# Optimization experiments

Measured on AMD Instinct MI355X. Metric: run time of the kernel, lower is better.

Reference implementation:

```python
import jax, jax.numpy as jnp
import numpy as np

NY, NU, NH = 8, 8, 256
T, NB = 2048, 64


def setup_inputs() -> dict:
    key = jax.random.key(0)
    ks = jax.random.split(key, 10)
    return {
        "_y0": jax.random.normal(ks[0], (NB, NY), dtype=jnp.float32),
        "_U": jax.random.normal(ks[1], (T, NB, NU), dtype=jnp.float32),
        "lmbd_cont_real": jax.random.uniform(ks[2], (NH // 2,), dtype=jnp.float32),
        "lmbd_cont_imag": jax.random.uniform(ks[3], (NH // 2,), dtype=jnp.float32),
        "B": jax.random.normal(ks[4], (NH, NU), dtype=jnp.float32) / np.sqrt(NU).astype(np.float32),
        "multiplier_on_B": jnp.zeros((NH,), dtype=jnp.float32),
        "W_y2x": jax.random.normal(ks[5], (NH, NY), dtype=jnp.float32) / np.sqrt(NY).astype(np.float32),
        "b_y2x": jax.random.normal(ks[6], (NH,), dtype=jnp.float32) * 0.01,
        "W_x2y": jax.random.normal(ks[7], (NY, NH), dtype=jnp.float32) / np.sqrt(NH).astype(np.float32),
        "b_x2y": jax.random.normal(ks[8], (NY,), dtype=jnp.float32) * 0.01,
    }


def reference(_y0, _U, lmbd_cont_real, lmbd_cont_imag, B, multiplier_on_B,
              W_y2x, b_y2x, W_x2y, b_x2y):
    H2 = lmbd_cont_real.shape[0]
    # input drive: (T, NB, NH)
    Bu = jnp.einsum('tbu,hu->tbh', _U, B) * jnp.exp(multiplier_on_B)
    # stable complex-conjugate-pair eigenvalues
    r = jnp.exp(-jnp.abs(lmbd_cont_real))
    theta = (jnp.pi / 2) * lmbd_cont_imag
    re = r * jnp.cos(theta)
    im = r * jnp.sin(theta)
    # initial state from y0
    x0 = _y0 @ W_y2x.T + b_y2x  # (NB, NH)

    def step(x, bu):
        x1, x2 = x[:, :H2], x[:, H2:]
        # A = [[diag(re), -diag(im)], [diag(im), diag(re)]]; x <- x A^T + bu
        nx = jnp.concatenate([re * x1 - im * x2, im * x1 + re * x2], axis=1) + bu
        return nx, nx

    _, X = jax.lax.scan(step, x0, Bu)  # X: (T, NB, NH)
    Y = X @ W_x2y.T + b_x2y  # (T, NB, NY)
    return Y
```

## Files before the change

### kernel.cpp

```cpp
#include <hip/hip_runtime.h>
#include <math.h>

#define T_   2048
#define NB_  64
#define NU_  8
#define NY_  8
#define NH_  256
#define H2_  128
#define CCH  64
#define LCH  32

static const float PI_HALF = 1.5707963267948966f;

typedef _Float16 half8  __attribute__((ext_vector_type(8)));
typedef __fp16   fp16x2 __attribute__((ext_vector_type(2)));
typedef float    f32x4  __attribute__((ext_vector_type(4)));

#define OFF_M     16384
#define OFF_CBUF  147456
#define OFF_INIT  4341760

__global__ __launch_bounds__(128) void k_scanM(
    const float* __restrict__ U, const float* __restrict__ bx2y,
    const float* __restrict__ lr, const float* __restrict__ li,
    const float* __restrict__ B, const float* __restrict__ mult,
    const float* __restrict__ Wx2y,
    char* __restrict__ ws, float* __restrict__ c_buf,
    float* __restrict__ Y)
{
    const int bi  = blockIdx.x;
    const int tid = threadIdx.x;

    if (bi < 256) {
        uint32_t* M32 = (uint32_t*)(ws + OFF_M);
        const int R = bi, dlt = R >> 3, y = R & 7;
        const int h = tid;
        const float e = (float)(dlt + 1);
        float r  = expf(-e * fabsf(lr[h]));
        float an = e * PI_HALF * li[h];
        float c = r * cosf(an), sn = r * sinf(an);
        float W1 = Wx2y[y*NH_ + h];
        float W2 = Wx2y[y*NH_ + h + H2_];
        float Mre = fmaf(W1, c,  W2 * sn);
        float Mim = fmaf(W2, c, -W1 * sn);
        union { fp16x2 h2; uint32_t u32; } pk;
        pk.h2 = __builtin_amdgcn_cvt_pkrtz(Mre, Mim);
        M32[R*128 + h] = pk.u32;
        return;
    }

    const int kb  = bi - 256;
    const int k   = kb >> 6;
    const int b   = kb & 63;
    const int h   = tid;
    const int w   = tid >> 6;
    const int l   = tid & 63;
    const int row = l & 15;
    const int kg  = (l >> 4) & 3;

    float4 lam;
    {
        float a_ = fabsf(lr[h]);
        float r_ = expf(-a_);
        float th = PI_HALF * li[h];
        float re = r_ * cosf(th), im = r_ * sinf(th);
        lam = make_float4(re, im, -im, re);
    }
    float B1[NU_], B2[NU_];
    {
        float s1 = expf(mult[h]), s2 = expf(mult[h + H2_]);
        const float4* bp1 = (const float4*)(B + h*NU_);
        const float4* bp2 = (const float4*)(B + (h + H2_)*NU_);
        float4 a0 = bp1[0], a1 = bp1[1], a2 = bp2[0], a3 = bp2[1];
        B1[0]=a0.x*s1; B1[1]=a0.y*s1; B1[2]=a0.z*s1; B1[3]=a0.w*s1;
        B1[4]=a1.x*s1; B1[5]=a1.y*s1; B1[6]=a1.z*s1; B1[7]=a1.w*s1;
        B2[0]=a2.x*s2; B2[1]=a2.y*s2; B2[2]=a2.z*s2; B2[3]=a2.w*s2;
        B2[4]=a3.x*s2; B2[5]=a3.y*s2; B2[6]=a3.z*s2; B2[7]=a3.w*s2;
    }
    half8 wf[4];
    #pragma unroll
    for (int q2 = 0; q2 < 4; q2++) {
        const int q = 4*w + q2;
        union { uint32_t u[4]; half8 h8; } fu;
        if (row < 8) {
            const float4 wa = *(const float4*)(Wx2y + row*NH_ + q*16 + kg*4);
            const float4 wb = *(const float4*)(Wx2y + row*NH_ + q*16 + kg*4 + H2_);
            union { fp16x2 h2; uint32_t u32; } p;
            p.h2 = __builtin_amdgcn_cvt_pkrtz(wa.x, wb.x); fu.u[0] = p.u32;
            p.h2 = __builtin_amdgcn_cvt_pkrtz(wa.y, wb.y); fu.u[1] = p.u32;
            p.h2 = __builtin_amdgcn_cvt_pkrtz(wa.z, wb.z); fu.u[2] = p.u32;
            p.h2 = __builtin_amdgcn_cvt_pkrtz(wa.w, wb.w); fu.u[3] = p.u32;
        } else {
            fu.u[0]=0; fu.u[1]=0; fu.u[2]=0; fu.u[3]=0;
        }
        wf[q2] = fu.h8;
    }
    const float bias = bx2y[tid & 7];

    __shared__ float    uS[LCH*NU_];
    __shared__ _Float16 xS[16*256];
    __shared__ float    pS[4*132];
    uint32_t* xS32 = (uint32_t*)xS;

    if (tid < 64) {
        ((float4*)uS)[tid] =
            *(const float4*)(U + ((size_t)(k*LCH + (tid>>1))*NB_ + b)*NU_ + (tid&1)*4);
    }
    __syncthreads();

    float x1 = 0.f, x2 = 0.f;
    const int g = h >> 2;

    for (int s = 0; s < 2; s++) {
        #pragma unroll 4
        for (int t16 = 0; t16 < 16; t16++) {
            const int t = s*16 + t16;
            float4 u0 = ((const float4*)uS)[2*t+0];
            float4 u1 = ((const float4*)uS)[2*t+1];
            float u[NU_] = {u0.x,u0.y,u0.z,u0.w,u1.x,u1.y,u1.z,u1.w};
            float bu1=0.f, bu2=0.f;
            #pragma unroll
            for (int i = 0; i < NU_; i++) {
                bu1 = fmaf(u[i], B1[i], bu1);
                bu2 = fmaf(u[i], B2[i], bu2);
            }
            float n1 = fmaf(lam.x, x1, fmaf(lam.z, x2, bu1));
            float n2 = fmaf(lam.y, x1, fmaf(lam.w, x2, bu2));
            x1 = n1; x2 = n2;

            union { fp16x2 h2; uint32_t u32; } pk;
            pk.h2 = __builtin_amdgcn_cvt_pkrtz(x1, x2);
            xS32[t16*128 + ((g ^ t16) & 31)*4 + (h & 3)] = pk.u32;
        }
        __syncthreads();

        f32x4 acc = {0.f,0.f,0.f,0.f};
        #pragma unroll
        for (int q2 = 0; q2 < 4; q2++) {
            const int q = 4*w + q2;
            const int p = ((q << 2) + kg) ^ row;
            const half8* ap = (const half8*)(xS + (row << 8) + (p << 3));
            acc = __builtin_amdgcn_mfma_f32_16x16x32_f16(*ap, wf[q2], acc, 0, 0, 0);
        }
        #pragma unroll
        for (int r = 0; r < 4; r++) pS[r*132 + w*64 + l] = acc[r];
        __syncthreads();

        {
            const int t  = tid >> 3, y = tid & 7;
            const int ls = ((t >> 2) << 4) + y;
            const int rg = t & 3;
            float sum = pS[rg*132 + ls] + pS[rg*132 + 64 + ls];
            Y[((size_t)(k*LCH + s*16 + t)*NB_ + b)*NY_ + y] = sum + bias;
        }
    }

    *(float2*)(c_buf + (size_t)(k*NB_ + b)*(H2_*2) + 2*h) = make_float2(x1, x2);
}

__global__ __launch_bounds__(64) void k_prefix(
    const float* __restrict__ y0, const float* __restrict__ Wy2x,
    const float* __restrict__ by2x,
    const float* __restrict__ lr, const float* __restrict__ li,
    const float* __restrict__ c_buf, uint32_t* __restrict__ initT)
{
    const int g = blockIdx.x*64 + threadIdx.x;
    const int b = g >> 7;
    const int h = g & 127;

    float x1 = by2x[h], x2 = by2x[h+H2_];
    #pragma unroll
    for (int y = 0; y < NY_; y++) {
        float yy = y0[b*NY_ + y];
        x1 = fmaf(yy, Wy2x[h*NY_ + y],        x1);
        x2 = fmaf(yy, Wy2x[(h+H2_)*NY_ + y],  x2);
    }

    const float a_  = fabsf(lr[h]);
    const float rL  = expf(-(float)LCH * a_);
    const float thL = (float)LCH * PI_HALF * li[h];
    const float reL = rL * cosf(thL), imL = rL * sinf(thL);

    #pragma unroll 8
    for (int k = 0; k < CCH; k++) {
        float2 c = *(const float2*)(c_buf + (size_t)k*16384 + b*256 + 2*h);
        union { fp16x2 hh; uint32_t u32; } pk;
        pk.hh = __builtin_amdgcn_cvt_pkrtz(x1, x2);
        initT[(size_t)k*8192 + b*128 + h] = pk.u32;
        float n1 = fmaf(reL, x1, fmaf(-imL, x2, c.x));
        float n2 = fmaf(imL, x1, fmaf( reL, x2, c.y));
        x1 = n1; x2 = n2;
    }
}

__global__ __launch_bounds__(256) void k_corr(
    const _Float16* __restrict__ M, const uint32_t* __restrict__ initT,
    float* __restrict__ Y)
{
    const int bi   = blockIdx.x;
    const int k    = bi >> 3;
    const int half = (bi >> 2) & 1;
    const int rtg  = bi & 3;
    const int tid  = threadIdx.x;
    const int w    = tid >> 6, l = tid & 63;
    const int lane16 = l & 15, kg = l >> 4;

    __shared__ _Float16 bS[32*264];
    {
        uint32_t* bS32 = (uint32_t*)bS;
        const int r = tid >> 3, seg = tid & 7;
        const uint32_t* src = initT + (size_t)k*8192 + (half*32 + r)*128 + seg*16;
        uint32_t* dst = bS32 + r*132 + seg*16;
        ((uint4*)dst)[0] = ((const uint4*)src)[0];
        ((uint4*)dst)[1] = ((const uint4*)src)[1];
        ((uint4*)dst)[2] = ((const uint4*)src)[2];
        ((uint4*)dst)[3] = ((const uint4*)src)[3];
    }
    __syncthreads();

    const int R0 = rtg*64 + w*16;
    half8 af[8];
    #pragma unroll
    for (int q = 0; q < 8; q++)
        af[q] = *(const half8*)(M + (size_t)(R0 + lane16)*256 + q*32 + kg*8);

    f32x4 acc0 = {0.f,0.f,0.f,0.f}, acc1 = {0.f,0.f,0.f,0.f};
    #pragma unroll
    for (int q = 0; q < 8; q++) {
        const half8* b0 = (const half8*)(bS + ( 0 + lane16)*264 + q*32 + kg*8);
        const half8* b1 = (const half8*)(bS + (16 + lane16)*264 + q*32 + kg*8);
        acc0 = __builtin_amdgcn_mfma_f32_16x16x32_f16(af[q], *b0, acc0, 0, 0, 0);
        acc1 = __builtin_amdgcn_mfma_f32_16x16x32_f16(af[q], *b1, acc1, 0, 0, 0);
    }

    const int t  = k*LCH + (R0 >> 3) + (kg >> 1);
    const int y0 = (kg & 1) * 4;
    float4* yp0 = (float4*)(Y + ((size_t)t*NB_ + half*32 +  0 + lane16)*NY_ + y0);
    float4* yp1 = (float4*)(Y + ((size_t)t*NB_ + half*32 + 16 + lane16)*NY_ + y0);
    float4 o0 = *yp0, o1 = *yp1;
    o0.x += acc0[0]; o0.y += acc0[1]; o0.z += acc0[2]; o0.w += acc0[3];
    o1.x += acc1[0]; o1.y += acc1[1]; o1.z += acc1[2]; o1.w += acc1[3];
    *yp0 = o0; *yp1 = o1;
}

extern "C" void kernel_launch(void* const* d_in, const int* in_sizes, int n_in,
                              void* d_out, int out_size, void* d_ws, size_t ws_size,
                              hipStream_t stream) {
    const float* y0   = (const float*)d_in[0];
    const float* U    = (const float*)d_in[1];
    const float* lr   = (const float*)d_in[2];
    const float* li   = (const float*)d_in[3];
    const float* B    = (const float*)d_in[4];
    const float* mult = (const float*)d_in[5];
    const float* Wy2x = (const float*)d_in[6];
    const float* by2x = (const float*)d_in[7];
    const float* Wx2y = (const float*)d_in[8];
    const float* bx2y = (const float*)d_in[9];
    float* Y = (float*)d_out;

    char*     ws    = (char*)d_ws;
    float*    c_buf = (float*)(ws + OFF_CBUF);
    uint32_t* initT = (uint32_t*)(ws + OFF_INIT);
    const _Float16* Mf = (const _Float16*)(ws + OFF_M);

    k_scanM <<<256 + CCH*NB_, 128, 0, stream>>>(U, bx2y, lr, li, B, mult, Wx2y,
                                                ws, c_buf, Y);
    k_prefix<<<(NB_*H2_)/64, 64, 0, stream>>>(y0, Wy2x, by2x, lr, li, c_buf, initT);
    k_corr  <<<CCH*8, 256, 0, stream>>>(Mf, initT, Y);
}
```

Measured before the change: 103.4 us.

## Merge prefix and correction kernels, parallelize chunk prefix with segmented scan

The serial 64-step chunk-carry prefix is split into 8 segments of 8 chunks per chain. Each segment is computed locally, then combined using the 8-chunk power of the eigenvalue. The prefix and correction kernels are fused into one launch: the first 256 blocks compute initial states, then every block spins on a global atomic counter before running the MFMA correction. This removes one launch and shortens the sequential dependency chain. The cost is redundant c_buf reads and a grid-wide spin barrier, which depends on all 512 blocks being co-resident.

```diff
diff --git a/kernel.cpp b/kernel.cpp
--- a/kernel.cpp
+++ b/kernel.cpp
@@ -16,6 +16,7 @@
 typedef __fp16   fp16x2 __attribute__((ext_vector_type(2)));
 typedef float    f32x4  __attribute__((ext_vector_type(4)));
 
+#define OFF_CNT   8
 #define OFF_M     16384
 #define OFF_CBUF  147456
 #define OFF_INIT  4341760
@@ -30,6 +31,10 @@
 {
     const int bi  = blockIdx.x;
     const int tid = threadIdx.x;
+
+    if (bi == 0 && tid == 0) {
+        *(volatile int*)(ws + OFF_CNT) = 0;
+    }
 
     if (bi < 256) {
         uint32_t* M32 = (uint32_t*)(ws + OFF_M);
@@ -158,54 +163,97 @@
     *(float2*)(c_buf + (size_t)(k*NB_ + b)*(H2_*2) + 2*h) = make_float2(x1, x2);
 }
 
-__global__ __launch_bounds__(64) void k_prefix(
+__global__ __launch_bounds__(256, 2) void k_pc(
     const float* __restrict__ y0, const float* __restrict__ Wy2x,
     const float* __restrict__ by2x,
     const float* __restrict__ lr, const float* __restrict__ li,
-    const float* __restrict__ c_buf, uint32_t* __restrict__ initT)
+    const float* __restrict__ c_buf, const _Float16* __restrict__ M,
+    uint32_t* __restrict__ initT, float* __restrict__ Y,
+    int* __restrict__ done)
 {
-    const int g = blockIdx.x*64 + threadIdx.x;
-    const int b = g >> 7;
-    const int h = g & 127;
-
-    float x1 = by2x[h], x2 = by2x[h+H2_];
-    #pragma unroll
-    for (int y = 0; y < NY_; y++) {
-        float yy = y0[b*NY_ + y];
-        x1 = fmaf(yy, Wy2x[h*NY_ + y],        x1);
-        x2 = fmaf(yy, Wy2x[(h+H2_)*NY_ + y],  x2);
-    }
-
-    const float a_  = fabsf(lr[h]);
-    const float rL  = expf(-(float)LCH * a_);
-    const float thL = (float)LCH * PI_HALF * li[h];
-    const float reL = rL * cosf(thL), imL = rL * sinf(thL);
-
-    #pragma unroll 8
-    for (int k = 0; k < CCH; k++) {
-        float2 c = *(const float2*)(c_buf + (size_t)k*16384 + b*256 + 2*h);
-        union { fp16x2 hh; uint32_t u32; } pk;
-        pk.hh = __builtin_amdgcn_cvt_pkrtz(x1, x2);
-        initT[(size_t)k*8192 + b*128 + h] = pk.u32;
-        float n1 = fmaf(reL, x1, fmaf(-imL, x2, c.x));
-        float n2 = fmaf(imL, x1, fmaf( reL, x2, c.y));
-        x1 = n1; x2 = n2;
-    }
-}
-
-__global__ __launch_bounds__(256) void k_corr(
-    const _Float16* __restrict__ M, const uint32_t* __restrict__ initT,
-    float* __restrict__ Y)
-{
-    const int bi   = blockIdx.x;
+    const int bi  = blockIdx.x;
+    const int tid = threadIdx.x;
+
+    __shared__ float2   Pseg[32][8];
+    __shared__ _Float16 bS[32*264];
+
+    if (bi < 256) {
+        const int chain = (bi << 5) + (tid >> 3);
+        const int seg   = tid & 7;
+        const int b = chain >> 7, h = chain & 127;
+
+        const float a_  = fabsf(lr[h]);
+        const float liv = li[h];
+        const float rL  = expf(-(float)LCH * a_);
+        const float thL = (float)LCH * PI_HALF * liv;
+        const float reL = rL * cosf(thL), imL = rL * sinf(thL);
+        const float r8  = expf(-(float)(8*LCH) * a_);
+        const float th8 = (float)(8*LCH) * PI_HALF * liv;
+        const float re8 = r8 * cosf(th8), im8 = r8 * sinf(th8);
+
+        float p1 = 0.f, p2 = 0.f;
+        #pragma unroll
+        for (int i = 0; i < 8; i++) {
+            const int k = (seg << 3) + i;
+            float2 c = *(const float2*)(c_buf + (size_t)k*16384 + b*256 + 2*h);
+            float n1 = fmaf(reL, p1, fmaf(-imL, p2, c.x));
+            float n2 = fmaf(imL, p1, fmaf( reL, p2, c.y));
+            p1 = n1; p2 = n2;
+        }
+        Pseg[tid >> 3][seg] = make_float2(p1, p2);
+
+        float x1 = by2x[h], x2 = by2x[h + H2_];
+        #pragma unroll
+        for (int y = 0; y < NY_; y++) {
+            float yy = y0[b*NY_ + y];
+            x1 = fmaf(yy, Wy2x[h*NY_ + y],        x1);
+            x2 = fmaf(yy, Wy2x[(h+H2_)*NY_ + y],  x2);
+        }
+        __syncthreads();
+
+        #pragma unroll
+        for (int j = 0; j < 7; j++) {
+            if (j < seg) {
+                float2 Pj = Pseg[tid >> 3][j];
+                float n1 = fmaf(re8, x1, fmaf(-im8, x2, Pj.x));
+                float n2 = fmaf(im8, x1, fmaf( re8, x2, Pj.y));
+                x1 = n1; x2 = n2;
+            }
+        }
+
+        #pragma unroll
+        for (int i = 0; i < 8; i++) {
+            const int k = (seg << 3) + i;
+            union { fp16x2 hh; uint32_t u32; } pk;
+            pk.hh = __builtin_amdgcn_cvt_pkrtz(x1, x2);
+            initT[(size_t)k*8192 + b*128 + h] = pk.u32;
+            float2 c = *(const float2*)(c_buf + (size_t)k*16384 + b*256 + 2*h);
+            float n1 = fmaf(reL, x1, fmaf(-imL, x2, c.x));
+            float n2 = fmaf(imL, x1, fmaf( reL, x2, c.y));
+            x1 = n1; x2 = n2;
+        }
+
+        __threadfence();
+        __syncthreads();
+        if (tid == 0)
+            __hip_atomic_fetch_add(done, 1, __ATOMIC_RELEASE,
+                                   __HIP_MEMORY_SCOPE_AGENT);
+    }
+
+    if (tid == 0) {
+        while (__hip_atomic_load(done, __ATOMIC_ACQUIRE,
+                                 __HIP_MEMORY_SCOPE_AGENT) < 256)
+            __builtin_amdgcn_s_sleep(4);
+    }
+    __syncthreads();
+    __threadfence();
+
     const int k    = bi >> 3;
     const int half = (bi >> 2) & 1;
     const int rtg  = bi & 3;
-    const int tid  = threadIdx.x;
     const int w    = tid >> 6, l = tid & 63;
     const int lane16 = l & 15, kg = l >> 4;
 
-    __shared__ _Float16 bS[32*264];
     {
         uint32_t* bS32 = (uint32_t*)bS;
         const int r = tid >> 3, seg = tid & 7;
@@ -234,9 +282,9 @@
     }
 
     const int t  = k*LCH + (R0 >> 3) + (kg >> 1);
-    const int y0 = (kg & 1) * 4;
-    float4* yp0 = (float4*)(Y + ((size_t)t*NB_ + half*32 +  0 + lane16)*NY_ + y0);
-    float4* yp1 = (float4*)(Y + ((size_t)t*NB_ + half*32 + 16 + lane16)*NY_ + y0);
+    const int y0i = (kg & 1) * 4;
+    float4* yp0 = (float4*)(Y + ((size_t)t*NB_ + half*32 +  0 + lane16)*NY_ + y0i);
+    float4* yp1 = (float4*)(Y + ((size_t)t*NB_ + half*32 + 16 + lane16)*NY_ + y0i);
     float4 o0 = *yp0, o1 = *yp1;
     o0.x += acc0[0]; o0.y += acc0[1]; o0.z += acc0[2]; o0.w += acc0[3];
     o1.x += acc1[0]; o1.y += acc1[1]; o1.z += acc1[2]; o1.w += acc1[3];
@@ -262,9 +310,10 @@
     float*    c_buf = (float*)(ws + OFF_CBUF);
     uint32_t* initT = (uint32_t*)(ws + OFF_INIT);
     const _Float16* Mf = (const _Float16*)(ws + OFF_M);
+    int*      done  = (int*)(ws + OFF_CNT);
 
     k_scanM <<<256 + CCH*NB_, 128, 0, stream>>>(U, bx2y, lr, li, B, mult, Wx2y,
                                                 ws, c_buf, Y);
-    k_prefix<<<(NB_*H2_)/64, 64, 0, stream>>>(y0, Wy2x, by2x, lr, li, c_buf, initT);
-    k_corr  <<<CCH*8, 256, 0, stream>>>(Mf, initT, Y);
+    k_pc    <<<CCH*8, 256, 0, stream>>>(y0, Wy2x, by2x, lr, li, c_buf, Mf,
+                                        initT, Y, done);
 }
```

After: 184.8 us. +78.7%, slower.
